# Optimization experiments

Measured on AMD Instinct MI355X. Metric: run time of the kernel, lower is better.

## Reference

```python
import jax, jax.numpy as jnp
import numpy as np

B = 2
NUM_EDGES = 50000          # line-graph nodes per sample
N = B * NUM_EDGES          # total nodes in batched graph
E = 400000                 # connectivity edges (before self-loops)
F_IN = 16                  # num_edge_features
TDIM = 64                  # time_embedding_dim
H, C = 4, 32               # heads, hidden_channels
HC = H * C                 # 128
NL_EXTRA = 3               # num_layers - 1
NCLASS = 2
THETA = 1.0
MAX_TIME = 1000.0
NEG_SLOPE = 0.2            # GATv2 leaky_relu slope (PyG default)

def _p(key, shape, s=0.05):
    return jax.random.normal(key, shape, dtype=jnp.float32) * s

def setup_inputs() -> dict:
    key = jax.random.key(0)
    ks = jax.random.split(key, 16)
    return {
        "x": jax.random.normal(ks[0], (N, F_IN), dtype=jnp.float32),
        "edge_index": jax.random.randint(ks[1], (2, E), 0, N, dtype=jnp.int32),
        "t": jax.random.randint(ks[2], (B,), 0, 1000, dtype=jnp.int32),
        "tW0": _p(ks[3], (TDIM, TDIM)), "tb0": jnp.zeros((TDIM,), jnp.float32),
        "tW1": _p(ks[4], (TDIM, TDIM)), "tb1": jnp.zeros((TDIM,), jnp.float32),
        "c0_Wl": _p(ks[5], (F_IN + TDIM, HC)), "c0_bl": jnp.zeros((HC,), jnp.float32),
        "c0_Wr": _p(ks[6], (F_IN + TDIM, HC)), "c0_br": jnp.zeros((HC,), jnp.float32),
        "c0_att": _p(ks[7], (H, C)), "c0_bias": jnp.zeros((HC,), jnp.float32),
        "r0_W": _p(ks[8], (F_IN + TDIM, HC)), "r0_b": jnp.zeros((HC,), jnp.float32),
        "cWl": _p(ks[9], (NL_EXTRA, HC, HC)),
        "cWr": _p(ks[10], (NL_EXTRA, HC, HC)),
        "catt": _p(ks[11], (NL_EXTRA, H, C)),
        "rW": _p(ks[12], (NL_EXTRA, HC, HC)), "rb": jnp.zeros((NL_EXTRA, HC), jnp.float32),
        "fdW": _p(ks[13], (HC, C)), "fdb": jnp.zeros((C,), jnp.float32),
        "acW": _p(ks[14], (C, NCLASS)), "acb": jnp.zeros((NCLASS,), jnp.float32),
    }

def _timestep_embedding(t):
    # Fairseq-style sinusoidal embedding, matches get_timestep_embedding
    ts = t.astype(jnp.float32) * (1000.0 / MAX_TIME)
    half = TDIM // 2
    freqs = jnp.exp(jnp.arange(half, dtype=jnp.float32) * (-jnp.log(10000.0) / (half - 1)))
    ang = ts[:, None] * freqs[None, :]
    return jnp.concatenate([jnp.sin(ang), jnp.cos(ang)], axis=1)  # [B, TDIM]

def _gatv2(x, Wl, bl, Wr, br, att, src, dst):
    # PyG GATv2Conv, concat=True, add_self_loops already in src/dst
    xl = x @ Wl
    xr = x @ Wr
    if bl is not None:
        xl = xl + bl
    if br is not None:
        xr = xr + br
    xl = xl.reshape(N, H, C)
    xr = xr.reshape(N, H, C)
    g = jax.nn.leaky_relu(xl[src] + xr[dst], NEG_SLOPE)          # [Etot, H, C]
    e = jnp.einsum('ehc,hc->eh', g, att)                          # [Etot, H]
    m = jax.ops.segment_max(e, dst, num_segments=N)
    ex = jnp.exp(e - m[dst])
    denom = jax.ops.segment_sum(ex, dst, num_segments=N)
    alpha = ex / denom[dst]
    out = jax.ops.segment_sum(alpha[:, :, None] * xl[src], dst, num_segments=N)
    return out.reshape(N, HC)

def reference(x, edge_index, t, tW0, tb0, tW1, tb1, c0_Wl, c0_bl, c0_Wr, c0_br,
              c0_att, c0_bias, r0_W, r0_b, cWl, cWr, catt, rW, rb,
              fdW, fdb, acW, acb):
    loops = jnp.arange(N, dtype=edge_index.dtype)
    src = jnp.concatenate([edge_index[0], loops])
    dst = jnp.concatenate([edge_index[1], loops])
    te = jax.nn.silu(_timestep_embedding(t) @ tW0 + tb0)
    te = jax.nn.silu(te @ tW1 + tb1)
    te = jnp.repeat(te, NUM_EDGES, axis=0)                        # repeat_interleave
    h = jnp.concatenate([x, te], axis=1)                          # [N, F_IN+TDIM]
    res = jax.nn.relu(h @ r0_W + r0_b)
    h = THETA * jax.nn.relu(_gatv2(h, c0_Wl, c0_bl, c0_Wr, c0_br, c0_att, src, dst) + c0_bias) + res
    for i in range(NL_EXTRA):
        res = jax.nn.relu(h @ rW[i] + rb[i])
        h = THETA * jax.nn.relu(_gatv2(h, cWl[i], None, cWr[i], None, catt[i], src, dst)) + res
    logits = (h @ fdW + fdb) @ acW + acb
    return logits.reshape(B, NUM_EDGES, NCLASS)
```

## Files before the change

### kernel.cpp

```cpp
#include <hip/hip_runtime.h>
#include <stdint.h>

#define NN 100000
#define EE 400000
#define NEDGE 50000
#define NBLK ((NN + 1023) / 1024)

typedef unsigned short u16;
typedef unsigned int u32;
typedef __attribute__((ext_vector_type(8))) __bf16 v8bf;
typedef __attribute__((ext_vector_type(4))) float v4f;

__device__ __forceinline__ float bf2f(u16 u) {
    return (float)__builtin_bit_cast(__bf16, u);
}
__device__ __forceinline__ u16 f2bf(float f) {
    __bf16 b = (__bf16)f;
    return __builtin_bit_cast(u16, b);
}
__device__ __forceinline__ void unpack8(const int4& v, float* f) {
    u32 a = (u32)v.x, b = (u32)v.y, c = (u32)v.z, d = (u32)v.w;
    f[0] = bf2f((u16)(a & 0xffff)); f[1] = bf2f((u16)(a >> 16));
    f[2] = bf2f((u16)(b & 0xffff)); f[3] = bf2f((u16)(b >> 16));
    f[4] = bf2f((u16)(c & 0xffff)); f[5] = bf2f((u16)(c >> 16));
    f[6] = bf2f((u16)(d & 0xffff)); f[7] = bf2f((u16)(d >> 16));
}

struct WPtrs { const float* p[12]; int K[12]; };

__global__ __launch_bounds__(256) void k_setup(WPtrs wp, u16* __restrict__ Wp,
        const int* __restrict__ t,
        const float* __restrict__ tW0, const float* __restrict__ tb0,
        const float* __restrict__ tW1, const float* __restrict__ tb1,
        float* __restrict__ te_out,
        const float* __restrict__ fdW, const float* __restrict__ fdb,
        const float* __restrict__ acW, const float* __restrict__ acb,
        float* __restrict__ Wf, float* __restrict__ bfu) {
    __shared__ float emb[2][64];
    __shared__ float u1[2][64];
    int b = blockIdx.x, tid = threadIdx.x;
    if (b < 768) {
        int idx = b * 256 + tid;
        int m = idx >> 14;
        int r = idx & 16383;
        int j = r & 7;
        int lane = (r >> 3) & 63;
        int fragid = r >> 9;
        int nt = fragid & 3;
        int ks = (fragid >> 2) & 3;
        int wc = fragid >> 4;
        int k = ks * 32 + ((lane >> 4) << 3) + j;
        int col = wc * 64 + nt * 16 + (lane & 15);
        float f = (k < wp.K[m]) ? wp.p[m][k * 128 + col] : 0.0f;
        Wp[idx] = f2bf(f);
    } else if (b == 768) {
        if (tid < 128) {
            int bb = tid >> 6, j = tid & 63;
            float ts = (float)t[bb];
            int jj = (j < 32) ? j : (j - 32);
            float fr = expf((float)jj * (-logf(10000.0f) / 31.0f));
            float ang = ts * fr;
            emb[bb][j] = (j < 32) ? sinf(ang) : cosf(ang);
        }
        __syncthreads();
        if (tid < 128) {
            int bb = tid >> 6, j = tid & 63;
            float s = tb0[j];
            for (int k = 0; k < 64; ++k) s += emb[bb][k] * tW0[k * 64 + j];
            s = s / (1.0f + expf(-s));
            u1[bb][j] = s;
        }
        __syncthreads();
        if (tid < 128) {
            int bb = tid >> 6, j = tid & 63;
            float s2 = tb1[j];
            for (int k = 0; k < 64; ++k) s2 += u1[bb][k] * tW1[k * 64 + j];
            s2 = s2 / (1.0f + expf(-s2));
            te_out[bb * 64 + j] = s2;
        }
    } else {
        int r = tid >> 1, c = tid & 1;
        float s = 0.f;
        for (int k = 0; k < 32; ++k) s += fdW[r * 32 + k] * acW[k * 2 + c];
        Wf[tid] = s;
        if (tid < 2) {
            float s2 = acb[tid];
            for (int k = 0; k < 32; ++k) s2 += fdb[k] * acW[k * 2 + tid];
            bfu[tid] = s2;
        }
    }
}

__global__ __launch_bounds__(256) void k_h0count(const float* __restrict__ x,
                                                 const float* __restrict__ te,
                                                 u16* __restrict__ h,
                                                 const int* __restrict__ ei,
                                                 int* __restrict__ deg) {
    int b = blockIdx.x, tid = threadIdx.x;
    if (b < 6250) {
        int idx = b * 256 + tid;
        int node = idx >> 4;
        int c8 = (idx & 15) << 3;
        u32 w_[4];
        if (c8 < 80) {
            const float* sp = (c8 < 16) ? (x + node * 16 + c8)
                                        : (te + ((node >= NEDGE) ? 64 : 0) + (c8 - 16));
#pragma unroll
            for (int i = 0; i < 4; ++i)
                w_[i] = (u32)f2bf(sp[2 * i]) | ((u32)f2bf(sp[2 * i + 1]) << 16);
        } else {
            w_[0] = w_[1] = w_[2] = w_[3] = 0;
        }
        int4 outv = make_int4((int)w_[0], (int)w_[1], (int)w_[2], (int)w_[3]);
        *reinterpret_cast<int4*>(h + node * 128 + c8) = outv;
    } else {
        int e = (b - 6250) * 256 + tid;
        if (e < EE) atomicAdd(&deg[ei[EE + e]], 1);
    }
}

__global__ __launch_bounds__(1024) void k_scan1(const int* __restrict__ deg,
                                                int* __restrict__ part, int* __restrict__ bsum) {
    __shared__ int wsum[16], woff[16];
    int tid = threadIdx.x, lane = tid & 63, wid = tid >> 6;
    int idx = blockIdx.x * 1024 + tid;
    int v = (idx < NN) ? deg[idx] : 0;
    int s = v;
#pragma unroll
    for (int off = 1; off < 64; off <<= 1) {
        int tv = __shfl_up(s, off);
        if (lane >= off) s += tv;
    }
    if (lane == 63) wsum[wid] = s;
    __syncthreads();
    if (wid == 0) {
        int ws_ = (lane < 16) ? wsum[lane] : 0;
        int t2 = ws_;
#pragma unroll
        for (int off = 1; off < 16; off <<= 1) {
            int tv = __shfl_up(t2, off);
            if (lane >= off) t2 += tv;
        }
        if (lane < 16) woff[lane] = t2 - ws_;
    }
    __syncthreads();
    int excl = woff[wid] + (s - v);
    if (idx < NN) part[idx] = excl;
    if (tid == 1023) bsum[blockIdx.x] = excl + v;
}

__global__ __launch_bounds__(256) void k_scan3(const int* __restrict__ part, const int* __restrict__ bsum,
                                               int* __restrict__ rowptr, int* __restrict__ cursor) {
    __shared__ int pre[NBLK + 1];
    __shared__ int sh_ws0;
    int tid = threadIdx.x;
    int lane = tid & 63, wid = tid >> 6;
    int v = 0, s = 0;
    if (tid < 128) {
        v = (tid < NBLK) ? bsum[tid] : 0;
        s = v;
#pragma unroll
        for (int off = 1; off < 64; off <<= 1) {
            int tv = __shfl_up(s, off);
            if (lane >= off) s += tv;
        }
        if (tid == 63) sh_ws0 = s;
    }
    __syncthreads();
    if (tid < 128) {
        int excl = (s - v) + (wid ? sh_ws0 : 0);
        if (tid <= NBLK) pre[tid] = excl;
    }
    __syncthreads();
    int idx = blockIdx.x * 256 + tid;
    if (idx > NN) return;
    int val = (idx == NN) ? pre[NBLK] : (part[idx] + pre[idx >> 10]);
    rowptr[idx] = val;
    if (idx < NN) cursor[idx] = val;
}

__global__ __launch_bounds__(256) void k_fill(const int* __restrict__ ei,
                                              int* __restrict__ cursor, int* __restrict__ colv) {
    int e = blockIdx.x * 256 + threadIdx.x;
    if (e >= EE) return;
    int s = ei[e], d = ei[EE + e];
    int pos = atomicAdd(&cursor[d], 1);
    colv[pos] = s;
}

__global__ __launch_bounds__(256) void k_gemm3(const u16* __restrict__ A,
                                               const u16* __restrict__ Wp,
                                               const float* __restrict__ b0,
                                               const float* __restrict__ b1,
                                               const float* __restrict__ b2,
                                               u16* __restrict__ xl, u16* __restrict__ xr,
                                               u16* __restrict__ res) {
    __shared__ __align__(16) u16 lA[64 * 128];
    __shared__ __align__(16) u16 lT[4][16][72];
    int tid = threadIdx.x;
    int lane = tid & 63, wid = tid >> 6;
    int wr = wid >> 1, wc = wid & 1;
    int row0 = blockIdx.x * 64;

#pragma unroll
    for (int i = 0; i < 4; ++i) {
        int chunk = i * 256 + wid * 64 + lane;
        int row = chunk >> 4;
        int cb = (chunk & 15) << 4;
        int scol = cb ^ ((row & 7) << 4);
        const u16* src = A + (size_t)(row0 + row) * 128 + (scol >> 1);
        u16* ldsbase = lA + (size_t)(i * 256 + wid * 64) * 8;
        __builtin_amdgcn_global_load_lds(
            (const __attribute__((address_space(1))) void*)src,
            (__attribute__((address_space(3))) void*)ldsbase, 16, 0, 0);
    }
    __syncthreads();

    const float* bptr[3] = {b0, b1, b2};
    u16* optr[3] = {xl, xr, res};

#pragma unroll
    for (int o = 0; o < 3; ++o) {
        v8bf bF[4][4];
        {
            const u16* wb = Wp + o * 16384 + ((wc * 16) * 64 + lane) * 8;
#pragma unroll
            for (int ks = 0; ks < 4; ++ks)
#pragma unroll
                for (int nt = 0; nt < 4; ++nt)
                    bF[ks][nt] = *reinterpret_cast<const v8bf*>(wb + (ks * 4 + nt) * 512);
        }

        v4f acc[2][4];
        v4f vzero = {0.f, 0.f, 0.f, 0.f};
#pragma unroll
        for (int m = 0; m < 2; ++m)
#pragma unroll
            for (int nt = 0; nt < 4; ++nt) acc[m][nt] = vzero;

#pragma unroll
        for (int ks = 0; ks < 4; ++ks) {
            v8bf aF[2];
#pragma unroll
            for (int m = 0; m < 2; ++m) {
                int row = wr * 32 + m * 16 + (lane & 15);
                int kb = ks * 64 + ((lane >> 4) << 4);
                int sb = kb ^ ((row & 7) << 4);
                aF[m] = *reinterpret_cast<const v8bf*>(reinterpret_cast<const char*>(lA) + row * 256 + sb);
            }
#pragma unroll
            for (int m = 0; m < 2; ++m)
#pragma unroll
                for (int nt = 0; nt < 4; ++nt)
                    acc[m][nt] = __builtin_amdgcn_mfma_f32_16x16x32_bf16(bF[ks][nt], aF[m], acc[m][nt], 0, 0, 0);
        }

        const float* bp = bptr[o];
        u16* op = optr[o];
        int relu = (o == 2);
        float4 bv[4];
#pragma unroll
        for (int nt = 0; nt < 4; ++nt)
            bv[nt] = bp ? *reinterpret_cast<const float4*>(bp + wc * 64 + nt * 16 + ((lane >> 4) << 2))
                        : make_float4(0.f, 0.f, 0.f, 0.f);

#pragma unroll
        for (int p = 0; p < 2; ++p) {
            int rl = lane & 15;
            int cl = (lane >> 4) << 2;
#pragma unroll
            for (int nt = 0; nt < 4; ++nt) {
                float v0 = acc[p][nt][0] + bv[nt].x;
                float v1 = acc[p][nt][1] + bv[nt].y;
                float v2 = acc[p][nt][2] + bv[nt].z;
                float v3 = acc[p][nt][3] + bv[nt].w;
                if (relu) {
                    v0 = fmaxf(v0, 0.f); v1 = fmaxf(v1, 0.f);
                    v2 = fmaxf(v2, 0.f); v3 = fmaxf(v3, 0.f);
                }
                int2 pk;
                pk.x = (int)((u32)f2bf(v0) | ((u32)f2bf(v1) << 16));
                pk.y = (int)((u32)f2bf(v2) | ((u32)f2bf(v3) << 16));
                *reinterpret_cast<int2*>(&lT[wid][rl][nt * 16 + cl]) = pk;
            }
#pragma unroll
            for (int i = 0; i < 2; ++i) {
                int rl2 = i * 8 + (lane >> 3);
                int4 v = *reinterpret_cast<const int4*>(&lT[wid][rl2][(lane & 7) * 8]);
                int grow = row0 + wr * 32 + p * 16 + rl2;
                if (grow < NN)
                    *reinterpret_cast<int4*>(op + grow * 128 + wc * 64 + (lane & 7) * 8) = v;
            }
        }
    }
}

__global__ __launch_bounds__(256) void k_gat(const u16* __restrict__ xl, const u16* __restrict__ xr,
                                             const float* __restrict__ att,
                                             const int* __restrict__ rowptr, const int* __restrict__ colv,
                                             const u16* __restrict__ res, const float* __restrict__ bias,
                                             u16* __restrict__ h,
                                             const float* __restrict__ Wf, const float* __restrict__ bfu,
                                             float* __restrict__ out) {
    int tid = threadIdx.x;
    int lane = tid & 63;
    int grp = lane >> 4;
    int s = lane & 15;
    int dst = blockIdx.x * 16 + (tid >> 6) * 4 + grp;
    if (dst >= NN) return;
    int c0 = s * 8;
    float av[8];
    *reinterpret_cast<float4*>(av) = *reinterpret_cast<const float4*>(att + c0);
    *reinterpret_cast<float4*>(av + 4) = *reinterpret_cast<const float4*>(att + c0 + 4);
    int4 xrv = *reinterpret_cast<const int4*>(xr + dst * 128 + c0);
    float xrf[8];
    unpack8(xrv, xrf);
    float den = 0.f;
    float acc[8] = {0.f, 0.f, 0.f, 0.f, 0.f, 0.f, 0.f, 0.f};
    int rbeg = rowptr[dst], rend = rowptr[dst + 1];
    for (int base = rbeg - 1; base < rend; base += 4) {
        int nv = rend - base; if (nv > 4) nv = 4;
        int4 xsv[4];
#pragma unroll
        for (int i = 0; i < 4; ++i) {
            if (i < nv) {
                int r = base + i;
                int src = (r < rbeg) ? dst : colv[r];
                xsv[i] = *reinterpret_cast<const int4*>(xl + (size_t)src * 128 + c0);
            }
        }
#pragma unroll
        for (int i = 0; i < 4; ++i) {
            if (i < nv) {
                float xs[8];
                unpack8(xsv[i], xs);
                float e = 0.f;
#pragma unroll
                for (int j = 0; j < 8; ++j) {
                    float gg = xs[j] + xrf[j];
                    gg = (gg > 0.f) ? gg : 0.2f * gg;
                    e = fmaf(gg, av[j], e);
                }
                e += __shfl_xor(e, 1, 4);
                e += __shfl_xor(e, 2, 4);
                float p = __expf(e);
                den += p;
#pragma unroll
                for (int j = 0; j < 8; ++j) acc[j] = fmaf(p, xs[j], acc[j]);
            }
        }
    }
    float inv = 1.0f / den;
    int4 rv = *reinterpret_cast<const int4*>(res + dst * 128 + c0);
    float rf[8];
    unpack8(rv, rf);
    float bvv[8] = {0.f, 0.f, 0.f, 0.f, 0.f, 0.f, 0.f, 0.f};
    if (bias) {
        *reinterpret_cast<float4*>(bvv) = *reinterpret_cast<const float4*>(bias + c0);
        *reinterpret_cast<float4*>(bvv + 4) = *reinterpret_cast<const float4*>(bias + c0 + 4);
    }
    float of[8];
#pragma unroll
    for (int j = 0; j < 8; ++j)
        of[j] = fmaxf(acc[j] * inv + bvv[j], 0.f) + rf[j];
    if (out) {
        float v0 = 0.f, v1 = 0.f;
#pragma unroll
        for (int j = 0; j < 8; ++j) {
            v0 = fmaf(of[j], Wf[(c0 + j) * 2], v0);
            v1 = fmaf(of[j], Wf[(c0 + j) * 2 + 1], v1);
        }
#pragma unroll
        for (int off = 1; off < 16; off <<= 1) {
            v0 += __shfl_xor(v0, off, 16);
            v1 += __shfl_xor(v1, off, 16);
        }
        if (s == 0) {
            float2 o = make_float2(v0 + bfu[0], v1 + bfu[1]);
            *reinterpret_cast<float2*>(out + dst * 2) = o;
        }
    } else {
        u32 ow[4];
#pragma unroll
        for (int j2 = 0; j2 < 4; ++j2)
            ow[j2] = (u32)f2bf(of[2 * j2]) | ((u32)f2bf(of[2 * j2 + 1]) << 16);
        *reinterpret_cast<int4*>(h + dst * 128 + c0) = make_int4((int)ow[0], (int)ow[1], (int)ow[2], (int)ow[3]);
    }
}

extern "C" void kernel_launch(void* const* d_in, const int* in_sizes, int n_in,
                              void* d_out, int out_size, void* d_ws, size_t ws_size,
                              hipStream_t stream) {
    const float* x      = (const float*)d_in[0];
    const int*   ei     = (const int*)d_in[1];
    const int*   t      = (const int*)d_in[2];
    const float* tW0    = (const float*)d_in[3];
    const float* tb0    = (const float*)d_in[4];
    const float* tW1    = (const float*)d_in[5];
    const float* tb1    = (const float*)d_in[6];
    const float* c0_Wl  = (const float*)d_in[7];
    const float* c0_bl  = (const float*)d_in[8];
    const float* c0_Wr  = (const float*)d_in[9];
    const float* c0_br  = (const float*)d_in[10];
    const float* c0_att = (const float*)d_in[11];
    const float* c0_bias= (const float*)d_in[12];
    const float* r0_W   = (const float*)d_in[13];
    const float* r0_b   = (const float*)d_in[14];
    const float* cWl    = (const float*)d_in[15];
    const float* cWr    = (const float*)d_in[16];
    const float* catt   = (const float*)d_in[17];
    const float* rW     = (const float*)d_in[18];
    const float* rb     = (const float*)d_in[19];
    const float* fdW    = (const float*)d_in[20];
    const float* fdb    = (const float*)d_in[21];
    const float* acW    = (const float*)d_in[22];
    const float* acb    = (const float*)d_in[23];
    (void)in_sizes; (void)n_in; (void)out_size; (void)ws_size;

    char* w = (char*)d_ws;
    const size_t HB = (size_t)NN * 128 * 2;
    float* te   = (float*)w;
    u16* h      = (u16*)(w + 4096);
    u16* xl     = (u16*)(w + 4096 + HB);
    u16* xr     = (u16*)(w + 4096 + 2 * HB);
    u16* res    = (u16*)(w + 4096 + 3 * HB);
    char* p     = w + 4096 + 4 * HB;
    int* deg    = (int*)(p);
    int* rowptr = (int*)(p + (1 << 19));
    int* cursor = (int*)(p + 2 * (1 << 19));
    int* colv   = (int*)(p + 3 * (1 << 19));
    int* part   = (int*)(p + 5 * (1 << 19));
    int* bsum   = (int*)(p + 6 * (1 << 19));
    u16* Wp     = (u16*)(p + 7 * (1 << 19));
    float* Wf   = (float*)(p + 8 * (1 << 19));
    float* bfu  = (float*)(p + 8 * (1 << 19) + 2048);

    WPtrs wp;
    wp.p[0] = c0_Wl; wp.p[1] = c0_Wr; wp.p[2] = r0_W;
    wp.K[0] = 80;    wp.K[1] = 80;    wp.K[2] = 80;
    for (int i = 0; i < 3; ++i) {
        wp.p[3 + 3 * i] = cWl + i * 16384;
        wp.p[4 + 3 * i] = cWr + i * 16384;
        wp.p[5 + 3 * i] = rW + i * 16384;
        wp.K[3 + 3 * i] = 128; wp.K[4 + 3 * i] = 128; wp.K[5 + 3 * i] = 128;
    }

    hipMemsetAsync(deg, 0, NN * sizeof(int), stream);
    k_setup<<<770, 256, 0, stream>>>(wp, Wp, t, tW0, tb0, tW1, tb1, te,
                                     fdW, fdb, acW, acb, Wf, bfu);
    k_h0count<<<6250 + 1563, 256, 0, stream>>>(x, te, h, ei, deg);
    k_scan1<<<NBLK, 1024, 0, stream>>>(deg, part, bsum);
    k_scan3<<<(NN + 256) / 256, 256, 0, stream>>>(part, bsum, rowptr, cursor);
    k_fill<<<(EE + 255) / 256, 256, 0, stream>>>(ei, cursor, colv);

    const int GB = (NN + 63) / 64;
    const int GG = (NN + 15) / 16;
    k_gemm3<<<GB, 256, 0, stream>>>(h, Wp, c0_bl, c0_br, r0_b, xl, xr, res);
    k_gat<<<GG, 256, 0, stream>>>(xl, xr, c0_att, rowptr, colv, res, c0_bias, h,
                                  nullptr, nullptr, nullptr);
    for (int i = 0; i < 3; ++i) {
        k_gemm3<<<GB, 256, 0, stream>>>(h, Wp + (3 + 3 * i) * 16384, nullptr, nullptr, rb + i * 128, xl, xr, res);
        k_gat<<<GG, 256, 0, stream>>>(xl, xr, catt + i * 128, rowptr, colv, res, nullptr, h,
                                      Wf, bfu, (i == 2) ? (float*)d_out : nullptr);
    }
}
```

Baseline: 432.6 us.

## Fuse GAT aggregation with next layer's projection GEMM via LDS tile

Adds a k_fgat kernel. It runs the GATv2 attention aggregation for a 64-row tile, writes the resulting hidden rows into a swizzled LDS tile, then runs the next layer's three projection GEMMs directly from LDS. This removes the global write and reread of h between layers and cuts the launch count. To avoid races the xl/xr/res buffers are ping-ponged. The cost is that each block now handles 64 destinations in four serial rounds, with more LDS per block, so the gather phase may have less parallelism.

```diff
diff --git a/kernel.cpp b/kernel.cpp
--- a/kernel.cpp
+++ b/kernel.cpp
@@ -188,37 +188,17 @@
     colv[pos] = s;
 }
 
-__global__ __launch_bounds__(256) void k_gemm3(const u16* __restrict__ A,
-                                               const u16* __restrict__ Wp,
-                                               const float* __restrict__ b0,
-                                               const float* __restrict__ b1,
-                                               const float* __restrict__ b2,
-                                               u16* __restrict__ xl, u16* __restrict__ xr,
-                                               u16* __restrict__ res) {
-    __shared__ __align__(16) u16 lA[64 * 128];
-    __shared__ __align__(16) u16 lT[4][16][72];
-    int tid = threadIdx.x;
-    int lane = tid & 63, wid = tid >> 6;
+__device__ __forceinline__ void gemm_from_lds(const u16* hT, u16* lTw,
+                                              const u16* __restrict__ Wp,
+                                              const float* __restrict__ b0,
+                                              const float* __restrict__ b1,
+                                              const float* __restrict__ b2,
+                                              u16* __restrict__ xl, u16* __restrict__ xr,
+                                              u16* __restrict__ res,
+                                              int lane, int wid, int row0) {
     int wr = wid >> 1, wc = wid & 1;
-    int row0 = blockIdx.x * 64;
-
-#pragma unroll
-    for (int i = 0; i < 4; ++i) {
-        int chunk = i * 256 + wid * 64 + lane;
-        int row = chunk >> 4;
-        int cb = (chunk & 15) << 4;
-        int scol = cb ^ ((row & 7) << 4);
-        const u16* src = A + (size_t)(row0 + row) * 128 + (scol >> 1);
-        u16* ldsbase = lA + (size_t)(i * 256 + wid * 64) * 8;
-        __builtin_amdgcn_global_load_lds(
-            (const __attribute__((address_space(1))) void*)src,
-            (__attribute__((address_space(3))) void*)ldsbase, 16, 0, 0);
-    }
-    __syncthreads();
-
     const float* bptr[3] = {b0, b1, b2};
     u16* optr[3] = {xl, xr, res};
-
 #pragma unroll
     for (int o = 0; o < 3; ++o) {
         v8bf bF[4][4];
@@ -230,14 +210,12 @@
                 for (int nt = 0; nt < 4; ++nt)
                     bF[ks][nt] = *reinterpret_cast<const v8bf*>(wb + (ks * 4 + nt) * 512);
         }
-
         v4f acc[2][4];
         v4f vzero = {0.f, 0.f, 0.f, 0.f};
 #pragma unroll
         for (int m = 0; m < 2; ++m)
 #pragma unroll
             for (int nt = 0; nt < 4; ++nt) acc[m][nt] = vzero;
-
 #pragma unroll
         for (int ks = 0; ks < 4; ++ks) {
             v8bf aF[2];
@@ -246,7 +224,7 @@
                 int row = wr * 32 + m * 16 + (lane & 15);
                 int kb = ks * 64 + ((lane >> 4) << 4);
                 int sb = kb ^ ((row & 7) << 4);
-                aF[m] = *reinterpret_cast<const v8bf*>(reinterpret_cast<const char*>(lA) + row * 256 + sb);
+                aF[m] = *reinterpret_cast<const v8bf*>(reinterpret_cast<const char*>(hT) + row * 256 + sb);
             }
 #pragma unroll
             for (int m = 0; m < 2; ++m)
@@ -254,7 +232,6 @@
                 for (int nt = 0; nt < 4; ++nt)
                     acc[m][nt] = __builtin_amdgcn_mfma_f32_16x16x32_bf16(bF[ks][nt], aF[m], acc[m][nt], 0, 0, 0);
         }
-
         const float* bp = bptr[o];
         u16* op = optr[o];
         int relu = (o == 2);
@@ -263,7 +240,6 @@
         for (int nt = 0; nt < 4; ++nt)
             bv[nt] = bp ? *reinterpret_cast<const float4*>(bp + wc * 64 + nt * 16 + ((lane >> 4) << 2))
                         : make_float4(0.f, 0.f, 0.f, 0.f);
-
 #pragma unroll
         for (int p = 0; p < 2; ++p) {
             int rl = lane & 15;
@@ -281,12 +257,12 @@
                 int2 pk;
                 pk.x = (int)((u32)f2bf(v0) | ((u32)f2bf(v1) << 16));
                 pk.y = (int)((u32)f2bf(v2) | ((u32)f2bf(v3) << 16));
-                *reinterpret_cast<int2*>(&lT[wid][rl][nt * 16 + cl]) = pk;
+                *reinterpret_cast<int2*>(lTw + rl * 72 + nt * 16 + cl) = pk;
             }
 #pragma unroll
             for (int i = 0; i < 2; ++i) {
                 int rl2 = i * 8 + (lane >> 3);
-                int4 v = *reinterpret_cast<const int4*>(&lT[wid][rl2][(lane & 7) * 8]);
+                int4 v = *reinterpret_cast<const int4*>(lTw + rl2 * 72 + (lane & 7) * 8);
                 int grow = row0 + wr * 32 + p * 16 + rl2;
                 if (grow < NN)
                     *reinterpret_cast<int4*>(op + grow * 128 + wc * 64 + (lane & 7) * 8) = v;
@@ -295,11 +271,126 @@
     }
 }
 
+__global__ __launch_bounds__(256) void k_gemm3(const u16* __restrict__ A,
+                                               const u16* __restrict__ Wp,
+                                               const float* __restrict__ b0,
+                                               const float* __restrict__ b1,
+                                               const float* __restrict__ b2,
+                                               u16* __restrict__ xl, u16* __restrict__ xr,
+                                               u16* __restrict__ res) {
+    __shared__ __align__(16) u16 lA[64 * 128];
+    __shared__ __align__(16) u16 lT[4][16 * 72];
+    int tid = threadIdx.x;
+    int lane = tid & 63, wid = tid >> 6;
+    int row0 = blockIdx.x * 64;
+#pragma unroll
+    for (int i = 0; i < 4; ++i) {
+        int chunk = i * 256 + wid * 64 + lane;
+        int row = chunk >> 4;
+        int cb = (chunk & 15) << 4;
+        int scol = cb ^ ((row & 7) << 4);
+        const u16* src = A + (size_t)(row0 + row) * 128 + (scol >> 1);
+        u16* ldsbase = lA + (size_t)(i * 256 + wid * 64) * 8;
+        __builtin_amdgcn_global_load_lds(
+            (const __attribute__((address_space(1))) void*)src,
+            (__attribute__((address_space(3))) void*)ldsbase, 16, 0, 0);
+    }
+    __syncthreads();
+    gemm_from_lds(lA, lT[wid], Wp, b0, b1, b2, xl, xr, res, lane, wid, row0);
+}
+
+__global__ __launch_bounds__(256) void k_fgat(const u16* __restrict__ xl_in, const u16* __restrict__ xr_in,
+                                              const u16* __restrict__ res_in,
+                                              const float* __restrict__ att,
+                                              const int* __restrict__ rowptr, const int* __restrict__ colv,
+                                              const float* __restrict__ bias,
+                                              const u16* __restrict__ Wp_next, const float* __restrict__ rb_next,
+                                              u16* __restrict__ xl_o, u16* __restrict__ xr_o,
+                                              u16* __restrict__ res_o) {
+    __shared__ __align__(16) u16 hT[64 * 128];
+    __shared__ __align__(16) u16 lT[4][16 * 72];
+    int tid = threadIdx.x;
+    int lane = tid & 63, wid = tid >> 6;
+    int row0 = blockIdx.x * 64;
+    int grp = lane >> 4, s = lane & 15;
+    int c0 = s * 8;
+
+    float av[8];
+    *reinterpret_cast<float4*>(av) = *reinterpret_cast<const float4*>(att + c0);
+    *reinterpret_cast<float4*>(av + 4) = *reinterpret_cast<const float4*>(att + c0 + 4);
+#pragma unroll 1
+    for (int round = 0; round < 4; ++round) {
+        int drow = wid * 16 + round * 4 + grp;
+        int dst = row0 + drow;
+        if (dst < NN) {
+            int4 xrv = *reinterpret_cast<const int4*>(xr_in + (size_t)dst * 128 + c0);
+            float xrf[8];
+            unpack8(xrv, xrf);
+            float den = 0.f;
+            float acc[8] = {0.f, 0.f, 0.f, 0.f, 0.f, 0.f, 0.f, 0.f};
+            int rbeg = rowptr[dst], rend = rowptr[dst + 1];
+            for (int base = rbeg - 1; base < rend; base += 4) {
+                int nv = rend - base; if (nv > 4) nv = 4;
+                int4 xsv[4];
+#pragma unroll
+                for (int i = 0; i < 4; ++i) {
+                    if (i < nv) {
+                        int r = base + i;
+                        int src = (r < rbeg) ? dst : colv[r];
+                        xsv[i] = *reinterpret_cast<const int4*>(xl_in + (size_t)src * 128 + c0);
+                    }
+                }
+#pragma unroll
+                for (int i = 0; i < 4; ++i) {
+                    if (i < nv) {
+                        float xs[8];
+                        unpack8(xsv[i], xs);
+                        float e = 0.f;
+#pragma unroll
+                        for (int j = 0; j < 8; ++j) {
+                            float gg = xs[j] + xrf[j];
+                            gg = (gg > 0.f) ? gg : 0.2f * gg;
+                            e = fmaf(gg, av[j], e);
+                        }
+                        e += __shfl_xor(e, 1, 4);
+                        e += __shfl_xor(e, 2, 4);
+                        float p = __expf(e);
+                        den += p;
+#pragma unroll
+                        for (int j = 0; j < 8; ++j) acc[j] = fmaf(p, xs[j], acc[j]);
+                    }
+                }
+            }
+            float inv = 1.0f / den;
+            int4 rv = *reinterpret_cast<const int4*>(res_in + (size_t)dst * 128 + c0);
+            float rf[8];
+            unpack8(rv, rf);
+            float bvv[8] = {0.f, 0.f, 0.f, 0.f, 0.f, 0.f, 0.f, 0.f};
+            if (bias) {
+                *reinterpret_cast<float4*>(bvv) = *reinterpret_cast<const float4*>(bias + c0);
+                *reinterpret_cast<float4*>(bvv + 4) = *reinterpret_cast<const float4*>(bias + c0 + 4);
+            }
+            u32 ow[4];
+#pragma unroll
+            for (int j2 = 0; j2 < 4; ++j2) {
+                float o0 = fmaxf(acc[2 * j2] * inv + bvv[2 * j2], 0.f) + rf[2 * j2];
+                float o1 = fmaxf(acc[2 * j2 + 1] * inv + bvv[2 * j2 + 1], 0.f) + rf[2 * j2 + 1];
+                ow[j2] = (u32)f2bf(o0) | ((u32)f2bf(o1) << 16);
+            }
+            int sb = (c0 * 2) ^ ((drow & 7) << 4);
+            *reinterpret_cast<int4*>(reinterpret_cast<char*>(hT) + drow * 256 + sb) =
+                make_int4((int)ow[0], (int)ow[1], (int)ow[2], (int)ow[3]);
+        }
+    }
+    __syncthreads();
+
+    gemm_from_lds(hT, lT[wid], Wp_next, nullptr, nullptr, rb_next, xl_o, xr_o, res_o, lane, wid, row0);
+}
+
 __global__ __launch_bounds__(256) void k_gat(const u16* __restrict__ xl, const u16* __restrict__ xr,
                                              const float* __restrict__ att,
                                              const int* __restrict__ rowptr, const int* __restrict__ colv,
-                                             const u16* __restrict__ res, const float* __restrict__ bias,
-                                             u16* __restrict__ h,
+                                             const u16* __restrict__ res,
                                              const float* __restrict__ Wf, const float* __restrict__ bfu,
                                              float* __restrict__ out) {
     int tid = threadIdx.x;
@@ -354,37 +445,24 @@
     int4 rv = *reinterpret_cast<const int4*>(res + dst * 128 + c0);
     float rf[8];
     unpack8(rv, rf);
-    float bvv[8] = {0.f, 0.f, 0.f, 0.f, 0.f, 0.f, 0.f, 0.f};
-    if (bias) {
-        *reinterpret_cast<float4*>(bvv) = *reinterpret_cast<const float4*>(bias + c0);
-        *reinterpret_cast<float4*>(bvv + 4) = *reinterpret_cast<const float4*>(bias + c0 + 4);
-    }
     float of[8];
 #pragma unroll
     for (int j = 0; j < 8; ++j)
-        of[j] = fmaxf(acc[j] * inv + bvv[j], 0.f) + rf[j];
-    if (out) {
-        float v0 = 0.f, v1 = 0.f;
-#pragma unroll
-        for (int j = 0; j < 8; ++j) {
-            v0 = fmaf(of[j], Wf[(c0 + j) * 2], v0);
-            v1 = fmaf(of[j], Wf[(c0 + j) * 2 + 1], v1);
-        }
-#pragma unroll
-        for (int off = 1; off < 16; off <<= 1) {
-            v0 += __shfl_xor(v0, off, 16);
-            v1 += __shfl_xor(v1, off, 16);
-        }
-        if (s == 0) {
-            float2 o = make_float2(v0 + bfu[0], v1 + bfu[1]);
-            *reinterpret_cast<float2*>(out + dst * 2) = o;
-        }
-    } else {
-        u32 ow[4];
-#pragma unroll
-        for (int j2 = 0; j2 < 4; ++j2)
-            ow[j2] = (u32)f2bf(of[2 * j2]) | ((u32)f2bf(of[2 * j2 + 1]) << 16);
-        *reinterpret_cast<int4*>(h + dst * 128 + c0) = make_int4((int)ow[0], (int)ow[1], (int)ow[2], (int)ow[3]);
+        of[j] = fmaxf(acc[j] * inv, 0.f) + rf[j];
+    float v0 = 0.f, v1 = 0.f;
+#pragma unroll
+    for (int j = 0; j < 8; ++j) {
+        v0 = fmaf(of[j], Wf[(c0 + j) * 2], v0);
+        v1 = fmaf(of[j], Wf[(c0 + j) * 2 + 1], v1);
+    }
+#pragma unroll
+    for (int off = 1; off < 16; off <<= 1) {
+        v0 += __shfl_xor(v0, off, 16);
+        v1 += __shfl_xor(v1, off, 16);
+    }
+    if (s == 0) {
+        float2 o = make_float2(v0 + bfu[0], v1 + bfu[1]);
+        *reinterpret_cast<float2*>(out + dst * 2) = o;
     }
 }
 
@@ -421,10 +499,13 @@
     const size_t HB = (size_t)NN * 128 * 2;
     float* te   = (float*)w;
     u16* h      = (u16*)(w + 4096);
-    u16* xl     = (u16*)(w + 4096 + HB);
-    u16* xr     = (u16*)(w + 4096 + 2 * HB);
-    u16* res    = (u16*)(w + 4096 + 3 * HB);
-    char* p     = w + 4096 + 4 * HB;
+    u16* xlA    = (u16*)(w + 4096 + HB);
+    u16* xrA    = (u16*)(w + 4096 + 2 * HB);
+    u16* resA   = (u16*)(w + 4096 + 3 * HB);
+    u16* xlB    = (u16*)(w + 4096 + 4 * HB);
+    u16* xrB    = (u16*)(w + 4096 + 5 * HB);
+    u16* resB   = (u16*)(w + 4096 + 6 * HB);
+    char* p     = w + 4096 + 7 * HB;
     int* deg    = (int*)(p);
     int* rowptr = (int*)(p + (1 << 19));
     int* cursor = (int*)(p + 2 * (1 << 19));
@@ -455,12 +536,13 @@
 
     const int GB = (NN + 63) / 64;
     const int GG = (NN + 15) / 16;
-    k_gemm3<<<GB, 256, 0, stream>>>(h, Wp, c0_bl, c0_br, r0_b, xl, xr, res);
-    k_gat<<<GG, 256, 0, stream>>>(xl, xr, c0_att, rowptr, colv, res, c0_bias, h,
-                                  nullptr, nullptr, nullptr);
-    for (int i = 0; i < 3; ++i) {
-        k_gemm3<<<GB, 256, 0, stream>>>(h, Wp + (3 + 3 * i) * 16384, nullptr, nullptr, rb + i * 128, xl, xr, res);
-        k_gat<<<GG, 256, 0, stream>>>(xl, xr, catt + i * 128, rowptr, colv, res, nullptr, h,
-                                      Wf, bfu, (i == 2) ? (float*)d_out : nullptr);
-    }
-}
+    k_gemm3<<<GB, 256, 0, stream>>>(h, Wp, c0_bl, c0_br, r0_b, xlA, xrA, resA);
+    k_fgat<<<GB, 256, 0, stream>>>(xlA, xrA, resA, c0_att, rowptr, colv, c0_bias,
+                                   Wp + 3 * 16384, rb + 0 * 128, xlB, xrB, resB);
+    k_fgat<<<GB, 256, 0, stream>>>(xlB, xrB, resB, catt + 0 * 128, rowptr, colv, nullptr,
+                                   Wp + 6 * 16384, rb + 1 * 128, xlA, xrA, resA);
+    k_fgat<<<GB, 256, 0, stream>>>(xlA, xrA, resA, catt + 1 * 128, rowptr, colv, nullptr,
+                                   Wp + 9 * 16384, rb + 2 * 128, xlB, xrB, resB);
+    k_gat<<<GG, 256, 0, stream>>>(xlB, xrB, catt + 2 * 128, rowptr, colv, resB,
+                                  Wf, bfu, (float*)d_out);
+}
```

Result: slower. 515.8 us (+19.2%).
